# Optimization experiments

Measured on AMD Instinct MI355X. Metric: run time of the kernel, lower is better.

Reference implementation:

```python
import jax, jax.numpy as jnp
import numpy as np
from math import sqrt

B, N, DIM_IN, DIM_K, DIM_V, NH = 4, 1024, 1024, 1024, 1024, 16


def setup_inputs() -> dict:
    key = jax.random.key(0)
    ks = jax.random.split(key, 5)
    x = jax.random.normal(ks[0], (B, N, DIM_IN), dtype=jnp.float32)
    y = jax.random.normal(ks[1], (B, N, DIM_IN), dtype=jnp.float32)
    # nn.Linear weights are (out_features, in_features); xavier-like scale
    s = 1.0 / sqrt(DIM_IN)
    Wq = jax.random.normal(ks[2], (DIM_K, DIM_IN), dtype=jnp.float32) * s
    Wk = jax.random.normal(ks[3], (DIM_K, DIM_IN), dtype=jnp.float32) * s
    Wv = jax.random.normal(ks[4], (DIM_V, DIM_IN), dtype=jnp.float32) * s
    return {"x": x, "y": y, "Wq": Wq, "Wk": Wk, "Wv": Wv}


def reference(x, y, Wq, Wk, Wv):
    b, n, _ = x.shape
    nh = NH
    dk = DIM_K // nh
    dv = DIM_V // nh
    norm = 1.0 / sqrt(dk)
    # project and split heads: (b, h, n, d)
    q = (x @ Wq.T).reshape(b, n, nh, dk).transpose(0, 2, 1, 3)
    k = (x @ Wk.T).reshape(b, n, nh, dk).transpose(0, 2, 1, 3)
    v = (y @ Wv.T).reshape(b, n, nh, dv).transpose(0, 2, 1, 3)
    scores = jnp.einsum("bhnd,bhmd->bhnm", q, k) * norm
    dist = jax.nn.softmax(scores, axis=-1)
    # contrast branch: softmax over (1 - dist)
    dist_a = jax.nn.softmax(1.0 - dist, axis=-1)
    c_att = jnp.einsum("bhnm,bhmd->bhnd", dist_a, v)
    c_att = c_att.transpose(0, 2, 1, 3).reshape(b, n, DIM_V)
    # normal branch: NOTE the original applies softmax to dist AGAIN
    dist2 = jax.nn.softmax(dist, axis=-1)
    att = jnp.einsum("bhnm,bhmd->bhnd", dist2, v)
    att = att.transpose(0, 2, 1, 3).reshape(b, n, DIM_V)
    return (c_att, att)
```

## Files before the change

### kernel.cpp

```cpp
#include <hip/hip_runtime.h>


typedef __attribute__((ext_vector_type(8))) short bf16x8;
typedef __attribute__((ext_vector_type(4))) float f32x4;
typedef __attribute__((ext_vector_type(4))) float float4v;
typedef __attribute__((ext_vector_type(2))) unsigned int uint2v;
typedef __attribute__((ext_vector_type(4))) unsigned short ushort4v;

#define DEVINL static __device__ __forceinline__

DEVINL unsigned f2bf_u(float f) {
  unsigned u = __float_as_uint(f);
  return (u + 0x7fffu + ((u >> 16) & 1u)) >> 16;
}
DEVINL unsigned short f2bf(float f) { return (unsigned short)f2bf_u(f); }
DEVINL unsigned pack2(float lo, float hi) { return f2bf_u(lo) | (f2bf_u(hi) << 16); }

DEVINL unsigned cvtpk(float lo, float hi) {
  unsigned r; asm("v_cvt_pk_bf16_f32 %0, %1, %2" : "=v"(r) : "v"(lo), "v"(hi)); return r;
}

DEVINL float fexp2(float x) {
  float r; asm("v_exp_f32 %0, %1" : "=v"(r) : "v"(x)); return r;
}

DEVINL void gload_lds16(const void* g, void* l) {
  __builtin_amdgcn_global_load_lds((const __attribute__((address_space(1))) unsigned int*)g,
                                   (__attribute__((address_space(3))) unsigned int*)l, 16, 0, 0);
}

DEVINL f32x4 mfma16(bf16x8 a, bf16x8 b, f32x4 c) {
  return __builtin_amdgcn_mfma_f32_16x16x32_bf16(a, b, c, 0, 0, 0);
}

DEVINL bf16x8 sq_frag(bf16x8 a) {
  union { bf16x8 h; unsigned u[4]; } ua; ua.h = a;
  union { unsigned u[4]; bf16x8 h; } ub;
#pragma unroll
  for (int d = 0; d < 4; ++d) {
    const float lo = __uint_as_float(ua.u[d] << 16);
    const float hi = __uint_as_float(ua.u[d] & 0xffff0000u);
    ub.u[d] = cvtpk(lo * lo, hi * hi);
  }
  return ub.h;
}

__global__ void cvt_all(const float* __restrict__ x, const float* __restrict__ y,
                        const float* __restrict__ wq, const float* __restrict__ wk,
                        const float* __restrict__ wv,
                        unsigned short* __restrict__ xb, unsigned short* __restrict__ yb,
                        unsigned short* __restrict__ wqb, unsigned short* __restrict__ wkb,
                        unsigned short* __restrict__ wvb) {
  long long e = (long long)blockIdx.x * 2048 + (long long)threadIdx.x * 8;
  const float* s; unsigned short* d; long long off;
  if (e < 4194304)       { s = x;  d = xb;  off = e; }
  else if (e < 8388608)  { s = y;  d = yb;  off = e - 4194304; }
  else if (e < 9437184)  { s = wq; d = wqb; off = e - 8388608; }
  else if (e < 10485760) { s = wk; d = wkb; off = e - 9437184; }
  else                   { s = wv; d = wvb; off = e - 10485760; }
  float4v a = *(const float4v*)(s + off);
  float4v b = *(const float4v*)(s + off + 4);
  ushort4v lo = { f2bf(a[0]), f2bf(a[1]), f2bf(a[2]), f2bf(a[3]) };
  ushort4v hi = { f2bf(b[0]), f2bf(b[1]), f2bf(b[2]), f2bf(b[3]) };
  *(ushort4v*)(d + off) = lo;
  *(ushort4v*)(d + off + 4) = hi;
}

__global__ __launch_bounds__(256, 3)
void gemm_proj(const unsigned short* __restrict__ xb, const unsigned short* __restrict__ yb,
               const unsigned short* __restrict__ wq, const unsigned short* __restrict__ wk,
               const unsigned short* __restrict__ wv,
               unsigned short* __restrict__ Qb, unsigned short* __restrict__ Kb,
               unsigned short* __restrict__ Vt) {
  const int z = blockIdx.z;
  const unsigned short* A  = (z == 2) ? yb : xb;
  const unsigned short* Bw = (z == 0) ? wq : ((z == 1) ? wk : wv);

  __shared__ unsigned short lA[128 * 32];
  __shared__ unsigned short lB[128 * 32];

  const int tid = threadIdx.x;
  const int w = tid >> 6, l = tid & 63;
  const int lq = l & 15, lg = l >> 4;
  const int tm = blockIdx.y, tn = blockIdx.x;

  const int srow = l >> 2;
  const int scol = (l & 3) * 8;
  const size_t arow0 = (size_t)tm * 128 + w * 16 + srow;
  const size_t brow0 = (size_t)tn * 128 + w * 16 + srow;
  const int wr = (w >> 1) * 64, wc = (w & 1) * 64;

  f32x4 zero4 = {0.f, 0.f, 0.f, 0.f};
  f32x4 acc[4][4];
#pragma unroll
  for (int m = 0; m < 4; ++m)
#pragma unroll
    for (int n = 0; n < 4; ++n) acc[m][n] = zero4;

  for (int k0 = 0; k0 < 1024; k0 += 32) {
    gload_lds16(A + arow0 * 1024 + k0 + scol,        &lA[w * 512]);
    gload_lds16(A + (arow0 + 64) * 1024 + k0 + scol, &lA[w * 512 + 2048]);
    gload_lds16(Bw + brow0 * 1024 + k0 + scol,        &lB[w * 512]);
    gload_lds16(Bw + (brow0 + 64) * 1024 + k0 + scol, &lB[w * 512 + 2048]);
    __syncthreads();
    bf16x8 af[4], bfr[4];
#pragma unroll
    for (int m = 0; m < 4; ++m) af[m]  = *(const bf16x8*)&lA[(wr + m * 16 + lq) * 32 + lg * 8];
#pragma unroll
    for (int n = 0; n < 4; ++n) bfr[n] = *(const bf16x8*)&lB[(wc + n * 16 + lq) * 32 + lg * 8];
#pragma unroll
    for (int m = 0; m < 4; ++m)
#pragma unroll
      for (int n = 0; n < 4; ++n)
        acc[m][n] = mfma16(af[m], bfr[n], acc[m][n]);
    __syncthreads();
  }

  if (z < 2) {
    unsigned short* O = (z == 0) ? Qb : Kb;
    const float scale = (z == 0) ? 0.18033688011116012f : 1.0f;
#pragma unroll
    for (int m = 0; m < 4; ++m)
#pragma unroll
      for (int n = 0; n < 4; ++n) {
        int row0 = tm * 128 + wr + m * 16 + lg * 4;
        int col  = tn * 128 + wc + n * 16 + lq;
#pragma unroll
        for (int j = 0; j < 4; ++j)
          O[(size_t)(row0 + j) * 1024 + col] = f2bf(acc[m][n][j] * scale);
      }
  } else {
#pragma unroll
    for (int m = 0; m < 4; ++m)
#pragma unroll
      for (int n = 0; n < 4; ++n) {
        int row0 = tm * 128 + wr + m * 16 + lg * 4;
        int col  = tn * 128 + wc + n * 16 + lq;
        int bb = row0 >> 10, n0 = row0 & 1023;
        uint2v p = { pack2(acc[m][n][0], acc[m][n][1]), pack2(acc[m][n][2], acc[m][n][3]) };
        *(uint2v*)(Vt + ((size_t)(bb * 1024 + col)) * 1024 + n0) = p;
      }
  }
}

DEVINL void stage_tileK512(const unsigned short* __restrict__ ghead, int m0,
                           unsigned short* tile, int tid) {
  const int row = tid >> 3;
  const int col16 = (tid & 7) ^ (row & 7);
  gload_lds16(ghead + (size_t)(m0 + row) * 1024 + col16 * 8, tile + (size_t)tid * 8);
}
DEVINL void stage_tileV512(const unsigned short* __restrict__ ghead, int m0,
                           unsigned short* tile, int tid) {
  const int row = tid >> 3;
  const int col16 = (tid & 7) ^ (row & 7);
  gload_lds16(ghead + (size_t)row * 1024 + m0 + col16 * 8, tile + (size_t)tid * 8);
}
DEVINL bf16x8 lds_rd(const unsigned short* tile, int r, int g) {
  return *(const bf16x8*)((const char*)tile + (r << 7) + ((g ^ (r & 7)) << 4));
}

__global__ __launch_bounds__(512, 4)
void attn_fused(const unsigned short* __restrict__ Qb, const unsigned short* __restrict__ Kb,
                const unsigned short* __restrict__ Vt, float* __restrict__ out) {
  __shared__ unsigned short Kl[2][4096];
  __shared__ unsigned short Vl[2][4096];
  __shared__ unsigned short Pl[8][1024];

  const int tid = threadIdx.x;
  const int w = tid >> 6, l = tid & 63;
  const int lq = l & 15, lg = l >> 4;

  const int orig = blockIdx.x;
  const int vid = (orig & 7) * 64 + (orig >> 3);
  const int tile = vid & 7;
  const int h = (vid >> 3) & 15;
  const int b = vid >> 7;
  const int qBase = tile * 128 + w * 16;

  const unsigned short* Khead = Kb + ((size_t)b << 20) + h * 64;
  const unsigned short* Vhead = Vt + ((size_t)(b * 1024 + h * 64)) * 1024;
  char* Pb = (char*)&Pl[w][0];

  bf16x8 qf[2];
#pragma unroll
  for (int kst = 0; kst < 2; ++kst)
    qf[kst] = *(const bf16x8*)(Qb + ((size_t)(b * 1024 + qBase + lq)) * 1024
                                  + h * 64 + kst * 32 + lg * 8);

  union { short s[8]; bf16x8 v; } onesU;
#pragma unroll
  for (int i = 0; i < 8; ++i) onesU.s[i] = (short)0x3F80;
  const bf16x8 ones = onesU.v;

  f32x4 zero4 = {0.f, 0.f, 0.f, 0.f};
  f32x4 m1[4], m2[4], mv[4];
  f32x4 s1a = zero4, s2a = zero4;
#pragma unroll
  for (int dvg = 0; dvg < 4; ++dvg) { m1[dvg] = zero4; m2[dvg] = zero4; mv[dvg] = zero4; }

  stage_tileK512(Khead, 0, Kl[0], tid);
  stage_tileV512(Vhead, 0, Vl[0], tid);
  __syncthreads();

  for (int mc = 0; mc < 16; ++mc) {
    if (mc < 15) {
      stage_tileK512(Khead, (mc + 1) * 64, Kl[(mc + 1) & 1], tid);
      stage_tileV512(Vhead, (mc + 1) * 64, Vl[(mc + 1) & 1], tid);
    }
    const unsigned short* Kt  = Kl[mc & 1];
    const unsigned short* Vtl = Vl[mc & 1];

#pragma unroll
    for (int sub = 0; sub < 4; ++sub) {
      const int r = sub * 16 + lq;
      bf16x8 ka0 = lds_rd(Kt, r, lg);
      bf16x8 ka1 = lds_rd(Kt, r, 4 + lg);
      f32x4 t = zero4;
      t = mfma16(ka0, qf[0], t);
      t = mfma16(ka1, qf[1], t);
      const float e0 = fexp2(fminf(t[0], 30.f)), e1 = fexp2(fminf(t[1], 30.f));
      const float e2 = fexp2(fminf(t[2], 30.f)), e3 = fexp2(fminf(t[3], 30.f));
      char* pp = Pb + lq * 128 + (((sub * 2 + (lg >> 1)) ^ (lq & 7)) << 4) + ((lg & 1) << 3);
      *(uint2v*)pp = (uint2v){ cvtpk(e0, e1), cvtpk(e2, e3) };
    }

#pragma unroll
    for (int kst2 = 0; kst2 < 2; ++kst2) {
      bf16x8 vf[4];
#pragma unroll
      for (int dvg = 0; dvg < 4; ++dvg)
        vf[dvg] = lds_rd(Vtl, dvg * 16 + lq, kst2 * 4 + lg);
      const int roff = lq * 128 + (((kst2 * 4 + lg) ^ (lq & 7)) << 4);
      bf16x8 a1 = *(const bf16x8*)(Pb + roff);
      bf16x8 a2 = sq_frag(a1);
      __builtin_amdgcn_s_setprio(1);
      s1a = mfma16(a1, ones, s1a);
      s2a = mfma16(a2, ones, s2a);
#pragma unroll
      for (int dvg = 0; dvg < 4; ++dvg) {
        mv[dvg] = mfma16(ones, vf[dvg], mv[dvg]);
        m1[dvg] = mfma16(a1, vf[dvg], m1[dvg]);
        m2[dvg] = mfma16(a2, vf[dvg], m2[dvg]);
      }
      __builtin_amdgcn_s_setprio(0);
    }
    __syncthreads();
  }

#pragma unroll
  for (int j = 0; j < 4; ++j) {
    const float Z  = s1a[j];
    const float iZ = 1.0f / Z;
    const float c2 = 0.5f * iZ * iZ;
    const float S2c2 = c2 * s2a[j];
    const float r2 = 1.0f / (1025.0f + S2c2);
    const float ra = 1.0f / (1023.0f + S2c2);
    const int nrow = qBase + lg * 4 + j;
    const size_t rb = ((size_t)(b * 1024 + nrow)) * 1024 + h * 64;
#pragma unroll
    for (int dvg = 0; dvg < 4; ++dvg) {
      const int dv = dvg * 16 + lq;
      const float A0 = mv[dvg][j];
      const float A1 = m1[dvg][j];
      const float A2 = m2[dvg][j];
      const float num2 = A0 + iZ * A1 + c2 * A2;
      const float numa = A0 - iZ * A1 + c2 * A2;
      out[rb + dv] = numa * ra;
      out[4194304 + rb + dv] = num2 * r2;
    }
  }
}

extern "C" void kernel_launch(void* const* d_in, const int* in_sizes, int n_in,
                              void* d_out, int out_size, void* d_ws, size_t ws_size,
                              hipStream_t stream) {
  const float* x  = (const float*)d_in[0];
  const float* y  = (const float*)d_in[1];
  const float* Wq = (const float*)d_in[2];
  const float* Wk = (const float*)d_in[3];
  const float* Wv = (const float*)d_in[4];
  float* out = (float*)d_out;
  char* ws = (char*)d_ws;
  const size_t MB = 1024 * 1024;
  unsigned short* xb  = (unsigned short*)(ws + 0 * MB);
  unsigned short* yb  = (unsigned short*)(ws + 8 * MB);
  unsigned short* wqb = (unsigned short*)(ws + 16 * MB);
  unsigned short* wkb = (unsigned short*)(ws + 18 * MB);
  unsigned short* wvb = (unsigned short*)(ws + 20 * MB);
  unsigned short* Qb  = (unsigned short*)(ws + 22 * MB);
  unsigned short* Kb  = (unsigned short*)(ws + 30 * MB);
  unsigned short* Vt  = (unsigned short*)(ws + 38 * MB);

  cvt_all<<<dim3(5632), dim3(256), 0, stream>>>(x, y, Wq, Wk, Wv, xb, yb, wqb, wkb, wvb);

  gemm_proj<<<dim3(8, 32, 3), dim3(256), 0, stream>>>(xb, yb, wqb, wkb, wvb, Qb, Kb, Vt);

  attn_fused<<<dim3(512), dim3(512), 0, stream>>>(Qb, Kb, Vt, out);
}
```

Measured before the change: 94.65 us.

## Remove redundant row-sum and V-sum MFMAs, reduce in registers and share via LDS

```diff
diff --git a/kernel.cpp b/kernel.cpp
--- a/kernel.cpp
+++ b/kernel.cpp
@@ -155,9 +155,6 @@
   const int col16 = (tid & 7) ^ (row & 7);
   gload_lds16(ghead + (size_t)row * 1024 + m0 + col16 * 8, tile + (size_t)tid * 8);
 }
-DEVINL bf16x8 lds_rd(const unsigned short* tile, int r, int g) {
-  return *(const bf16x8*)((const char*)tile + (r << 7) + ((g ^ (r & 7)) << 4));
-}
 
 __global__ __launch_bounds__(512, 4)
 void attn_fused(const unsigned short* __restrict__ Qb, const unsigned short* __restrict__ Kb,
@@ -165,6 +162,7 @@
   __shared__ unsigned short Kl[2][4096];
   __shared__ unsigned short Vl[2][4096];
   __shared__ unsigned short Pl[8][1024];
+  __shared__ float M0s[64];
 
   const int tid = threadIdx.x;
   const int w = tid >> 6, l = tid & 63;
@@ -192,9 +190,28 @@
   for (int i = 0; i < 8; ++i) onesU.s[i] = (short)0x3F80;
   const bf16x8 ones = onesU.v;
 
+  int offK[4][2], offPw[4];
+#pragma unroll
+  for (int sub = 0; sub < 4; ++sub) {
+    const int r = sub * 16 + lq;
+    offK[sub][0] = (r << 7) + ((lg ^ (r & 7)) << 4);
+    offK[sub][1] = (r << 7) + (((4 + lg) ^ (r & 7)) << 4);
+    offPw[sub] = lq * 128 + (((sub * 2 + (lg >> 1)) ^ (lq & 7)) << 4) + ((lg & 1) << 3);
+  }
+  int offV[2][4], offPr[2];
+#pragma unroll
+  for (int kst = 0; kst < 2; ++kst) {
+    offPr[kst] = lq * 128 + (((kst * 4 + lg) ^ (lq & 7)) << 4);
+#pragma unroll
+    for (int dvg = 0; dvg < 4; ++dvg) {
+      const int rv = dvg * 16 + lq;
+      offV[kst][dvg] = (rv << 7) + (((kst * 4 + lg) ^ (rv & 7)) << 4);
+    }
+  }
+
   f32x4 zero4 = {0.f, 0.f, 0.f, 0.f};
   f32x4 m1[4], m2[4], mv[4];
-  f32x4 s1a = zero4, s2a = zero4;
+  float zs1 = 0.f, zs2 = 0.f;
 #pragma unroll
   for (int dvg = 0; dvg < 4; ++dvg) { m1[dvg] = zero4; m2[dvg] = zero4; mv[dvg] = zero4; }
 
@@ -202,43 +219,45 @@
   stage_tileV512(Vhead, 0, Vl[0], tid);
   __syncthreads();
 
+#pragma unroll 2
   for (int mc = 0; mc < 16; ++mc) {
     if (mc < 15) {
       stage_tileK512(Khead, (mc + 1) * 64, Kl[(mc + 1) & 1], tid);
       stage_tileV512(Vhead, (mc + 1) * 64, Vl[(mc + 1) & 1], tid);
     }
-    const unsigned short* Kt  = Kl[mc & 1];
-    const unsigned short* Vtl = Vl[mc & 1];
+    const char* Kt  = (const char*)Kl[mc & 1];
+    const char* Vtl = (const char*)Vl[mc & 1];
 
 #pragma unroll
     for (int sub = 0; sub < 4; ++sub) {
-      const int r = sub * 16 + lq;
-      bf16x8 ka0 = lds_rd(Kt, r, lg);
-      bf16x8 ka1 = lds_rd(Kt, r, 4 + lg);
+      bf16x8 ka0 = *(const bf16x8*)(Kt + offK[sub][0]);
+      bf16x8 ka1 = *(const bf16x8*)(Kt + offK[sub][1]);
       f32x4 t = zero4;
       t = mfma16(ka0, qf[0], t);
       t = mfma16(ka1, qf[1], t);
       const float e0 = fexp2(fminf(t[0], 30.f)), e1 = fexp2(fminf(t[1], 30.f));
       const float e2 = fexp2(fminf(t[2], 30.f)), e3 = fexp2(fminf(t[3], 30.f));
-      char* pp = Pb + lq * 128 + (((sub * 2 + (lg >> 1)) ^ (lq & 7)) << 4) + ((lg & 1) << 3);
-      *(uint2v*)pp = (uint2v){ cvtpk(e0, e1), cvtpk(e2, e3) };
-    }
-
-#pragma unroll
-    for (int kst2 = 0; kst2 < 2; ++kst2) {
+      zs1 += (e0 + e1) + (e2 + e3);
+      zs2 += (e0 * e0 + e1 * e1) + (e2 * e2 + e3 * e3);
+      *(uint2v*)(Pb + offPw[sub]) = (uint2v){ cvtpk(e0, e1), cvtpk(e2, e3) };
+    }
+
+#pragma unroll
+    for (int kst = 0; kst < 2; ++kst) {
       bf16x8 vf[4];
 #pragma unroll
       for (int dvg = 0; dvg < 4; ++dvg)
-        vf[dvg] = lds_rd(Vtl, dvg * 16 + lq, kst2 * 4 + lg);
-      const int roff = lq * 128 + (((kst2 * 4 + lg) ^ (lq & 7)) << 4);
-      bf16x8 a1 = *(const bf16x8*)(Pb + roff);
+        vf[dvg] = *(const bf16x8*)(Vtl + offV[kst][dvg]);
+      bf16x8 a1 = *(const bf16x8*)(Pb + offPr[kst]);
       bf16x8 a2 = sq_frag(a1);
       __builtin_amdgcn_s_setprio(1);
-      s1a = mfma16(a1, ones, s1a);
-      s2a = mfma16(a2, ones, s2a);
+      if (w == 0) {
+#pragma unroll
+        for (int dvg = 0; dvg < 4; ++dvg)
+          mv[dvg] = mfma16(ones, vf[dvg], mv[dvg]);
+      }
 #pragma unroll
       for (int dvg = 0; dvg < 4; ++dvg) {
-        mv[dvg] = mfma16(ones, vf[dvg], mv[dvg]);
         m1[dvg] = mfma16(a1, vf[dvg], m1[dvg]);
         m2[dvg] = mfma16(a2, vf[dvg], m2[dvg]);
       }
@@ -247,26 +266,43 @@
     __syncthreads();
   }
 
+  if (w == 0 && lg == 0) {
+#pragma unroll
+    for (int dvg = 0; dvg < 4; ++dvg) M0s[dvg * 16 + lq] = mv[dvg][0];
+  }
+
+  zs1 += __shfl_xor(zs1, 16, 64); zs1 += __shfl_xor(zs1, 32, 64);
+  zs2 += __shfl_xor(zs2, 16, 64); zs2 += __shfl_xor(zs2, 32, 64);
+  const float iZ = 1.0f / zs1;
+  const float c2 = 0.5f * iZ * iZ;
+  const float S2c2 = c2 * zs2;
+  const float r2 = 1.0f / (1025.0f + S2c2);
+  const float ra = 1.0f / (1023.0f + S2c2);
+
+  __syncthreads();
+  float A0v[4];
+#pragma unroll
+  for (int dvg = 0; dvg < 4; ++dvg) A0v[dvg] = M0s[dvg * 16 + lq];
+
 #pragma unroll
   for (int j = 0; j < 4; ++j) {
-    const float Z  = s1a[j];
-    const float iZ = 1.0f / Z;
-    const float c2 = 0.5f * iZ * iZ;
-    const float S2c2 = c2 * s2a[j];
-    const float r2 = 1.0f / (1025.0f + S2c2);
-    const float ra = 1.0f / (1023.0f + S2c2);
+    const int src = lg * 4 + j;
+    const float iZj = __shfl(iZ, src, 64);
+    const float c2j = __shfl(c2, src, 64);
+    const float r2j = __shfl(r2, src, 64);
+    const float raj = __shfl(ra, src, 64);
     const int nrow = qBase + lg * 4 + j;
     const size_t rb = ((size_t)(b * 1024 + nrow)) * 1024 + h * 64;
 #pragma unroll
     for (int dvg = 0; dvg < 4; ++dvg) {
       const int dv = dvg * 16 + lq;
-      const float A0 = mv[dvg][j];
+      const float A0 = A0v[dvg];
       const float A1 = m1[dvg][j];
       const float A2 = m2[dvg][j];
-      const float num2 = A0 + iZ * A1 + c2 * A2;
-      const float numa = A0 - iZ * A1 + c2 * A2;
-      out[rb + dv] = numa * ra;
-      out[4194304 + rb + dv] = num2 * r2;
+      const float num2 = A0 + iZj * A1 + c2j * A2;
+      const float numa = A0 - iZj * A1 + c2j * A2;
+      out[rb + dv] = numa * raj;
+      out[4194304 + rb + dv] = num2 * r2j;
     }
   }
 }
```

New measurement: 156.7 us. 1.66x slower.
